# Performance work log

Measured on AMD Instinct MI355X. Metric: run time of the kernel, lower is better.

The kernel has to match this reference:

```python
import jax, jax.numpy as jnp
import numpy as np
from jax import lax

NEG = jnp.float32(-1e9)
POS = jnp.float32(1e9)


def _edt_sq(mask):
    """Exact squared Euclidean distance transform of a 2D boolean mask.

    mask: [H, W] bool, True = foreground (nonzero in scipy terms).
    Returns [H, W] float32 squared distance to nearest background (False) pixel.
    Felzenszwalb-Huttenlocher separable formulation:
      pass 1 (axis 0): 1D distance to nearest zero per column (O(H) via scans)
      pass 2 (axis 1): min-plus convolution with quadratic per row.
    """
    H, W = mask.shape
    zero = ~mask
    idx = jnp.broadcast_to(jnp.arange(H, dtype=jnp.float32)[:, None], (H, W))
    # index of last background pixel at-or-above, and next at-or-below, per column
    last0 = lax.associative_scan(jnp.maximum, jnp.where(zero, idx, NEG), axis=0)
    next0 = jnp.flip(
        lax.associative_scan(jnp.minimum, jnp.flip(jnp.where(zero, idx, POS), 0), axis=0), 0)
    d1 = jnp.minimum(idx - last0, next0 - idx)  # 1D distance along axis 0
    f = jnp.where(mask, d1 * d1, jnp.float32(0.0))  # squared axis-0 distance
    # pass 2: D[i, j] = min_j' f[i, j'] + (j - j')^2
    jq = jnp.arange(W, dtype=jnp.float32)
    q = (jq[:, None] - jq[None, :]) ** 2  # [W, W]
    def row_min(frow):  # frow: [W]
        return jnp.min(frow[None, :] + q, axis=1)  # [W]
    return lax.map(row_min, f)  # [H, W]


def setup_inputs() -> dict:
    key = jax.random.key(0)
    img = jax.random.uniform(key, (2048, 2048), dtype=jnp.float32)
    return {"img": img}


def reference(img) -> jnp.ndarray:
    mask = img > 0.5  # scipy: nonzero pixels are foreground
    d = jnp.sqrt(_edt_sq(mask))
    m = jnp.max(d)
    d = jnp.where(m > 0, d / m * 255.0, d)  # `if img.max() != 0: img = img/max*255`
    return d.astype(jnp.uint8)  # img.astype(np.uint8)
```

## Files before the change

### kernel.cpp

```cpp
#include <hip/hip_runtime.h>
#include <math.h>

typedef unsigned long long u64;

#define H 2048
#define W 2048
#define NWR 64
#define TILE 128
#define HALO 32
#define LW 192
#define LSTRIDE 193
#define DCLAMP 2900
#define NTHR 256
#define NBLK 1024

#define TAG_PACK  0x11C0FFEEu
#define TAG_FLAG2 0x22C0FFEEu
#define TAG_V     0x33C0FFEEull
#define TAG_F     0x44C0FFEEull

__device__ __attribute__((noinline)) int vfar_up(const unsigned* rmask, int col, int r, int ks) {
    for (int kk = ks - 2; kk >= 0; --kk) {
        unsigned w = rmask[kk * W + col];
        if (w) return r - (kk * 32 + (31 - __clz(w)));
    }
    return DCLAMP;
}
__device__ __attribute__((noinline)) int vfar_dn(const unsigned* rmask, int col, int r, int ks) {
    for (int kk = ks + 2; kk < NWR; ++kk) {
        unsigned w = rmask[kk * W + col];
        if (w) return (kk * 32 + (__ffs(w) - 1)) - r;
    }
    return DCLAMP;
}

__device__ __attribute__((noinline)) float f_from_mask(const unsigned* rmask, int col, int r) {
    int kw = r >> 5, b = r & 31;
    unsigned wm1 = (kw > 0)       ? rmask[(kw - 1) * W + col] : 0u;
    unsigned w0  =                  rmask[kw * W + col];
    unsigned wp1 = (kw < NWR - 1) ? rmask[(kw + 1) * W + col] : 0u;
    if ((w0 >> b) & 1u) return 0.0f;
    u64 A  = (u64)wm1 | ((u64)w0 << 32);
    u64 Bv = (u64)w0  | ((u64)wp1 << 32);
    int p = 32 + b;
    u64 Am = A & ((1ull << p) - 1ull);
    int da = Am ? (p - (63 - __clzll(Am))) : vfar_up(rmask, col, r, kw);
    u64 Bm = Bv >> (b + 1);
    int db = Bm ? __ffsll(Bm) : vfar_dn(rmask, col, r, kw);
    int d1 = min(min(da, db), DCLAMP);
    return (float)d1 * (float)d1;
}

__global__ void __launch_bounds__(NTHR, 4)
edt_one(const float* __restrict__ img, int* __restrict__ out,
        unsigned* __restrict__ rmask,
        unsigned* __restrict__ valid2, unsigned* __restrict__ flag2,
        u64* __restrict__ vcell, u64* __restrict__ flag) {
    __shared__ float ftile[32][LSTRIDE];
    __shared__ unsigned packbuf[TILE];
    __shared__ float smax[5];
    const int tid = threadIdx.x;
    const int c0 = blockIdx.x * TILE;
    const int ks = blockIdx.y;
    const int rbase = ks * 32;
    const int bid = ks * (W / TILE) + blockIdx.x;

    {
        const int half = tid >> 7;
        const int colp = tid & 127;
        const int rb = rbase + half * 16;
        unsigned pw = 0;
#pragma unroll
        for (int i = 0; i < 16; ++i)
            pw |= (img[(size_t)(rb + i) * W + c0 + colp] <= 0.5f ? 1u : 0u) << i;
        if (half) packbuf[colp] = pw;
        __syncthreads();
        if (!half) rmask[ks * W + c0 + colp] = pw | (packbuf[colp] << 16);
        __syncthreads();
    }

    if (tid == 0)
        __hip_atomic_store(&valid2[bid], TAG_PACK, __ATOMIC_RELEASE,
                           __HIP_MEMORY_SCOPE_AGENT);
    if (bid == 0) {
#pragma unroll
        for (int k = 0; k < NBLK / NTHR; ++k)
            while (__hip_atomic_load(&valid2[tid * (NBLK / NTHR) + k],
                                     __ATOMIC_RELAXED, __HIP_MEMORY_SCOPE_AGENT) != TAG_PACK)
                __builtin_amdgcn_s_sleep(2);
        __syncthreads();
        if (tid == 0)
            __hip_atomic_store(flag2, TAG_FLAG2, __ATOMIC_RELEASE,
                               __HIP_MEMORY_SCOPE_AGENT);
    } else if (tid == 0) {
        while (__hip_atomic_load(flag2, __ATOMIC_RELAXED,
                                 __HIP_MEMORY_SCOPE_AGENT) != TAG_FLAG2)
            __builtin_amdgcn_s_sleep(4);
    }
    __syncthreads();

    if (tid < LW) {
        int gc = c0 - HALO + tid;
        if (gc >= 0 && gc < W) {
            unsigned wm1 = (ks > 0)       ? rmask[(ks - 1) * W + gc] : 0u;
            unsigned w0  =                  rmask[ks * W + gc];
            unsigned wp1 = (ks < NWR - 1) ? rmask[(ks + 1) * W + gc] : 0u;
            u64 A  = (u64)wm1 | ((u64)w0 << 32);
            u64 Bv = (u64)w0  | ((u64)wp1 << 32);
#pragma unroll
            for (int i = 0; i < 32; ++i) {
                int p = 32 + i;
                u64 Am = A & ((1ull << p) - 1ull);
                int da = Am ? (p - (63 - __clzll(Am))) : vfar_up(rmask, gc, rbase + i, ks);
                u64 Bm = Bv >> (i + 1);
                int db = Bm ? __ffsll(Bm) : vfar_dn(rmask, gc, rbase + i, ks);
                int d1 = min(min(da, db), DCLAMP);
                float fd = (float)d1;
                ftile[i][tid] = ((w0 >> i) & 1u) ? 0.0f : fd * fd;
            }
        } else {
#pragma unroll
            for (int i = 0; i < 32; ++i)
                ftile[i][tid] = 1e9f;
        }
    }
    __syncthreads();

    const int i  = tid & 31;
    const int p  = tid >> 5;
    const int lc = HALO + p * 16;
    float reg[32];
#pragma unroll
    for (int k = 0; k < 32; ++k)
        reg[k] = ftile[i][lc - 8 + k];

    float res[16];
    float lmax = 0.0f;
#pragma unroll
    for (int m = 0; m < 16; ++m) {
        float best = reg[m + 8];
#pragma unroll
        for (int d = 1; d <= 8; ++d) {
            float q = (float)(d * d);
            best = fminf(best, reg[m + 8 - d] + q);
            best = fminf(best, reg[m + 8 + d] + q);
        }
        if (__builtin_expect(81.0f < best, 0)) {
            for (int d = 9; d <= HALO && (float)(d * d) < best; ++d) {
                float q = (float)(d * d);
                best = fminf(best, ftile[i][lc + m - d] + q);
                best = fminf(best, ftile[i][lc + m + d] + q);
            }
            if ((float)((HALO + 1) * (HALO + 1)) < best) {
                int r = rbase + i, jj = c0 + p * 16 + m;
                for (int d = HALO + 1; d < W && (float)(d * d) < best; ++d) {
                    float q = (float)(d * d);
                    int jm = jj - d, jp = jj + d;
                    if (jm >= 0) best = fminf(best, f_from_mask(rmask, jm, r) + q);
                    if (jp < W)  best = fminf(best, f_from_mask(rmask, jp, r) + q);
                }
            }
        }
        float rr = sqrtf(best);
        res[m] = rr;
        lmax = fmaxf(lmax, rr);
    }

    __syncthreads();
#pragma unroll
    for (int m = 0; m < 16; ++m)
        ftile[i][p * 16 + m] = res[m];

    for (int o = 32; o > 0; o >>= 1) lmax = fmaxf(lmax, __shfl_down(lmax, o, 64));
    if ((tid & 63) == 0) smax[1 + (tid >> 6)] = lmax;
    __syncthreads();

    if (tid == 0) {
        float bm = fmaxf(fmaxf(smax[1], smax[2]), fmaxf(smax[3], smax[4]));
        u64 v = (TAG_V << 32) | (u64)__float_as_uint(bm);
        __hip_atomic_store(&vcell[bid], v, __ATOMIC_RELEASE, __HIP_MEMORY_SCOPE_AGENT);
    }
    if (bid == 0) {
        float mv = 0.0f;
#pragma unroll
        for (int k = 0; k < NBLK / NTHR; ++k) {
            u64 v;
            while (((v = __hip_atomic_load(&vcell[tid * (NBLK / NTHR) + k],
                                           __ATOMIC_RELAXED, __HIP_MEMORY_SCOPE_AGENT))
                    >> 32) != TAG_V)
                __builtin_amdgcn_s_sleep(2);
            mv = fmaxf(mv, __uint_as_float((unsigned)v));
        }
        for (int o = 32; o > 0; o >>= 1) mv = fmaxf(mv, __shfl_down(mv, o, 64));
        if ((tid & 63) == 0) smax[1 + (tid >> 6)] = mv;
        __syncthreads();
        if (tid == 0) {
            float gm = fmaxf(fmaxf(smax[1], smax[2]), fmaxf(smax[3], smax[4]));
            smax[0] = gm;
            u64 v = (TAG_F << 32) | (u64)__float_as_uint(gm);
            __hip_atomic_store(flag, v, __ATOMIC_RELEASE, __HIP_MEMORY_SCOPE_AGENT);
        }
    } else if (tid == 0) {
        u64 v;
        while (((v = __hip_atomic_load(flag, __ATOMIC_RELAXED,
                                       __HIP_MEMORY_SCOPE_AGENT)) >> 32) != TAG_F)
            __builtin_amdgcn_s_sleep(4);
        smax[0] = __uint_as_float((unsigned)v);
    }
    __syncthreads();

    float m = smax[0];
    float scale = (m > 0.0f) ? 1.0f / m : 0.0f;
#pragma unroll
    for (int q = 0; q < 4; ++q) {
        int r  = (tid >> 5) + 8 * q;
        int c4 = (tid & 31) * 4;
        int o[4];
#pragma unroll
        for (int k = 0; k < 4; ++k) {
            float dv = ftile[r][c4 + k];
            float v = (m > 0.0f) ? (dv * scale * 255.0f) : dv;
            v = fminf(fmaxf(v, 0.0f), 255.0f);
            o[k] = (int)v;
        }
        *(int4*)(out + (size_t)(rbase + r) * W + c0 + c4) = make_int4(o[0], o[1], o[2], o[3]);
    }
}

extern "C" void kernel_launch(void* const* d_in, const int* in_sizes, int n_in,
                              void* d_out, int out_size, void* d_ws, size_t ws_size,
                              hipStream_t stream) {
    const float* img = (const float*)d_in[0];
    int* out = (int*)d_out;

    char* ws = (char*)d_ws;
    unsigned* rmask  = (unsigned*)ws;
    unsigned* valid2 = (unsigned*)(ws + 524288);
    unsigned* flag2  = (unsigned*)(ws + 524288 + 4096 + 128);
    u64*      vcell  = (u64*)(ws + 524288 + 8192);
    u64*      flag   = (u64*)(ws + 524288 + 8192 + 8192 + 128);

    edt_one<<<dim3(W / TILE, NWR), dim3(NTHR), 0, stream>>>(
        img, out, rmask, valid2, flag2, vcell, flag);
}
```

Before: 100.5 us.

## Drop packed-mask grid barrier and rebuild column bitmasks from the image per block

The kernel no longer packs the binary mask into a global bitmask array, so the first grid-wide barrier is gone. Each block now rebuilds the 32-row column bitmasks for its own row band, plus the bands above and below, straight from the float image. The rare far-distance fallbacks now scan image rows instead of packed words. This trades a global synchronisation for redundant image reads, about three times the rows plus the column halo per block. The max-reduction stores are also relaxed from release to relaxed ordering and the spin sleep is lengthened.

```diff
diff --git a/kernel.cpp b/kernel.cpp
--- a/kernel.cpp
+++ b/kernel.cpp
@@ -14,50 +14,34 @@
 #define NTHR 256
 #define NBLK 1024
 
-#define TAG_PACK  0x11C0FFEEu
-#define TAG_FLAG2 0x22C0FFEEu
-#define TAG_V     0x33C0FFEEull
-#define TAG_F     0x44C0FFEEull
-
-__device__ __attribute__((noinline)) int vfar_up(const unsigned* rmask, int col, int r, int ks) {
-    for (int kk = ks - 2; kk >= 0; --kk) {
-        unsigned w = rmask[kk * W + col];
-        if (w) return r - (kk * 32 + (31 - __clz(w)));
-    }
+#define TAG_V  0x33C0FFEEull
+#define TAG_F  0x44C0FFEEull
+
+__device__ __attribute__((noinline)) int vfar_up_img(const float* img, int col, int r, int rtop) {
+    for (int rr = rtop - 1; rr >= 0; --rr)
+        if (img[(size_t)rr * W + col] <= 0.5f) return r - rr;
     return DCLAMP;
 }
-__device__ __attribute__((noinline)) int vfar_dn(const unsigned* rmask, int col, int r, int ks) {
-    for (int kk = ks + 2; kk < NWR; ++kk) {
-        unsigned w = rmask[kk * W + col];
-        if (w) return (kk * 32 + (__ffs(w) - 1)) - r;
-    }
+__device__ __attribute__((noinline)) int vfar_dn_img(const float* img, int col, int r, int rbot) {
+    for (int rr = rbot + 1; rr < H; ++rr)
+        if (img[(size_t)rr * W + col] <= 0.5f) return rr - r;
     return DCLAMP;
 }
-
-__device__ __attribute__((noinline)) float f_from_mask(const unsigned* rmask, int col, int r) {
-    int kw = r >> 5, b = r & 31;
-    unsigned wm1 = (kw > 0)       ? rmask[(kw - 1) * W + col] : 0u;
-    unsigned w0  =                  rmask[kw * W + col];
-    unsigned wp1 = (kw < NWR - 1) ? rmask[(kw + 1) * W + col] : 0u;
-    if ((w0 >> b) & 1u) return 0.0f;
-    u64 A  = (u64)wm1 | ((u64)w0 << 32);
-    u64 Bv = (u64)w0  | ((u64)wp1 << 32);
-    int p = 32 + b;
-    u64 Am = A & ((1ull << p) - 1ull);
-    int da = Am ? (p - (63 - __clzll(Am))) : vfar_up(rmask, col, r, kw);
-    u64 Bm = Bv >> (b + 1);
-    int db = Bm ? __ffsll(Bm) : vfar_dn(rmask, col, r, kw);
-    int d1 = min(min(da, db), DCLAMP);
+__device__ __attribute__((noinline)) float f_from_img(const float* img, int col, int r) {
+    if (img[(size_t)r * W + col] <= 0.5f) return 0.0f;
+    int du = DCLAMP, dn = DCLAMP;
+    for (int dd = 1; r - dd >= 0; ++dd)
+        if (img[(size_t)(r - dd) * W + col] <= 0.5f) { du = dd; break; }
+    for (int dd = 1; r + dd < H; ++dd)
+        if (img[(size_t)(r + dd) * W + col] <= 0.5f) { dn = dd; break; }
+    int d1 = min(min(du, dn), DCLAMP);
     return (float)d1 * (float)d1;
 }
 
 __global__ void __launch_bounds__(NTHR, 4)
-edt_one(const float* __restrict__ img, int* __restrict__ out,
-        unsigned* __restrict__ rmask,
-        unsigned* __restrict__ valid2, unsigned* __restrict__ flag2,
-        u64* __restrict__ vcell, u64* __restrict__ flag) {
+edt_solo(const float* __restrict__ img, int* __restrict__ out,
+         u64* __restrict__ vcell, u64* __restrict__ flag) {
     __shared__ float ftile[32][LSTRIDE];
-    __shared__ unsigned packbuf[TILE];
     __shared__ float smax[5];
     const int tid = threadIdx.x;
     const int c0 = blockIdx.x * TILE;
@@ -65,55 +49,34 @@
     const int rbase = ks * 32;
     const int bid = ks * (W / TILE) + blockIdx.x;
 
-    {
-        const int half = tid >> 7;
-        const int colp = tid & 127;
-        const int rb = rbase + half * 16;
-        unsigned pw = 0;
-#pragma unroll
-        for (int i = 0; i < 16; ++i)
-            pw |= (img[(size_t)(rb + i) * W + c0 + colp] <= 0.5f ? 1u : 0u) << i;
-        if (half) packbuf[colp] = pw;
-        __syncthreads();
-        if (!half) rmask[ks * W + c0 + colp] = pw | (packbuf[colp] << 16);
-        __syncthreads();
-    }
-
-    if (tid == 0)
-        __hip_atomic_store(&valid2[bid], TAG_PACK, __ATOMIC_RELEASE,
-                           __HIP_MEMORY_SCOPE_AGENT);
-    if (bid == 0) {
-#pragma unroll
-        for (int k = 0; k < NBLK / NTHR; ++k)
-            while (__hip_atomic_load(&valid2[tid * (NBLK / NTHR) + k],
-                                     __ATOMIC_RELAXED, __HIP_MEMORY_SCOPE_AGENT) != TAG_PACK)
-                __builtin_amdgcn_s_sleep(2);
-        __syncthreads();
-        if (tid == 0)
-            __hip_atomic_store(flag2, TAG_FLAG2, __ATOMIC_RELEASE,
-                               __HIP_MEMORY_SCOPE_AGENT);
-    } else if (tid == 0) {
-        while (__hip_atomic_load(flag2, __ATOMIC_RELAXED,
-                                 __HIP_MEMORY_SCOPE_AGENT) != TAG_FLAG2)
-            __builtin_amdgcn_s_sleep(4);
-    }
-    __syncthreads();
-
     if (tid < LW) {
         int gc = c0 - HALO + tid;
         if (gc >= 0 && gc < W) {
-            unsigned wm1 = (ks > 0)       ? rmask[(ks - 1) * W + gc] : 0u;
-            unsigned w0  =                  rmask[ks * W + gc];
-            unsigned wp1 = (ks < NWR - 1) ? rmask[(ks + 1) * W + gc] : 0u;
+            unsigned wm1 = 0, w0 = 0, wp1 = 0;
+            if (ks > 0) {
+#pragma unroll
+                for (int i = 0; i < 32; ++i)
+                    wm1 |= (img[(size_t)(rbase - 32 + i) * W + gc] <= 0.5f ? 1u : 0u) << i;
+            }
+#pragma unroll
+            for (int i = 0; i < 32; ++i)
+                w0 |= (img[(size_t)(rbase + i) * W + gc] <= 0.5f ? 1u : 0u) << i;
+            if (ks < NWR - 1) {
+#pragma unroll
+                for (int i = 0; i < 32; ++i)
+                    wp1 |= (img[(size_t)(rbase + 32 + i) * W + gc] <= 0.5f ? 1u : 0u) << i;
+            }
             u64 A  = (u64)wm1 | ((u64)w0 << 32);
             u64 Bv = (u64)w0  | ((u64)wp1 << 32);
 #pragma unroll
             for (int i = 0; i < 32; ++i) {
                 int p = 32 + i;
                 u64 Am = A & ((1ull << p) - 1ull);
-                int da = Am ? (p - (63 - __clzll(Am))) : vfar_up(rmask, gc, rbase + i, ks);
+                int da = Am ? (p - (63 - __clzll(Am)))
+                            : vfar_up_img(img, gc, rbase + i, rbase - 32);
                 u64 Bm = Bv >> (i + 1);
-                int db = Bm ? __ffsll(Bm) : vfar_dn(rmask, gc, rbase + i, ks);
+                int db = Bm ? __ffsll(Bm)
+                            : vfar_dn_img(img, gc, rbase + i, rbase + 63);
                 int d1 = min(min(da, db), DCLAMP);
                 float fd = (float)d1;
                 ftile[i][tid] = ((w0 >> i) & 1u) ? 0.0f : fd * fd;
@@ -156,8 +119,8 @@
                 for (int d = HALO + 1; d < W && (float)(d * d) < best; ++d) {
                     float q = (float)(d * d);
                     int jm = jj - d, jp = jj + d;
-                    if (jm >= 0) best = fminf(best, f_from_mask(rmask, jm, r) + q);
-                    if (jp < W)  best = fminf(best, f_from_mask(rmask, jp, r) + q);
+                    if (jm >= 0) best = fminf(best, f_from_img(img, jm, r) + q);
+                    if (jp < W)  best = fminf(best, f_from_img(img, jp, r) + q);
                 }
             }
         }
@@ -178,7 +141,7 @@
     if (tid == 0) {
         float bm = fmaxf(fmaxf(smax[1], smax[2]), fmaxf(smax[3], smax[4]));
         u64 v = (TAG_V << 32) | (u64)__float_as_uint(bm);
-        __hip_atomic_store(&vcell[bid], v, __ATOMIC_RELEASE, __HIP_MEMORY_SCOPE_AGENT);
+        __hip_atomic_store(&vcell[bid], v, __ATOMIC_RELAXED, __HIP_MEMORY_SCOPE_AGENT);
     }
     if (bid == 0) {
         float mv = 0.0f;
@@ -198,13 +161,13 @@
             float gm = fmaxf(fmaxf(smax[1], smax[2]), fmaxf(smax[3], smax[4]));
             smax[0] = gm;
             u64 v = (TAG_F << 32) | (u64)__float_as_uint(gm);
-            __hip_atomic_store(flag, v, __ATOMIC_RELEASE, __HIP_MEMORY_SCOPE_AGENT);
+            __hip_atomic_store(flag, v, __ATOMIC_RELAXED, __HIP_MEMORY_SCOPE_AGENT);
         }
     } else if (tid == 0) {
         u64 v;
         while (((v = __hip_atomic_load(flag, __ATOMIC_RELAXED,
                                        __HIP_MEMORY_SCOPE_AGENT)) >> 32) != TAG_F)
-            __builtin_amdgcn_s_sleep(4);
+            __builtin_amdgcn_s_sleep(8);
         smax[0] = __uint_as_float((unsigned)v);
     }
     __syncthreads();
@@ -233,13 +196,8 @@
     const float* img = (const float*)d_in[0];
     int* out = (int*)d_out;
 
-    char* ws = (char*)d_ws;
-    unsigned* rmask  = (unsigned*)ws;
-    unsigned* valid2 = (unsigned*)(ws + 524288);
-    unsigned* flag2  = (unsigned*)(ws + 524288 + 4096 + 128);
-    u64*      vcell  = (u64*)(ws + 524288 + 8192);
-    u64*      flag   = (u64*)(ws + 524288 + 8192 + 8192 + 128);
-
-    edt_one<<<dim3(W / TILE, NWR), dim3(NTHR), 0, stream>>>(
-        img, out, rmask, valid2, flag2, vcell, flag);
-}
+    u64* vcell = (u64*)d_ws;
+    u64* flag  = (u64*)((char*)d_ws + 8192 + 128);
+
+    edt_solo<<<dim3(W / TILE, NWR), dim3(NTHR), 0, stream>>>(img, out, vcell, flag);
+}
```

Result: faster. 81.30 us (-19.1%).
